# Kernel optimization log

Hardware: AMD Instinct MI355X
Metric: run time of the kernel (lower is better)

Reference implementation:

```python
import jax, jax.numpy as jnp
import numpy as np

B, Q = 4096, 1024   # batch, time-series length
L, K = 64, 32       # num shapelets, shapelet length


def setup_inputs() -> dict:
    key = jax.random.key(0)
    k1, k2, k3, k4 = jax.random.split(key, 4)
    return {
        "ts": jax.random.normal(k1, (B, Q), dtype=jnp.float32),
        "shapelets": jax.random.normal(k2, (L, K), dtype=jnp.float32),
        "fc_w": jax.random.normal(k3, (2, L), dtype=jnp.float32) * 0.1,
        "fc_b": jax.random.normal(k4, (2,), dtype=jnp.float32) * 0.1,
    }


def reference(ts, shapelets, fc_w, fc_b):
    # Sliding-window mean squared distance, fused via the expansion
    #   mean((seg - s)^2) = (sum seg^2 - 2 seg.s + sum s^2) / K
    # which avoids materializing [B, L, S, K] windows.
    S = Q - K + 1  # number of segments

    # sliding sum of ts^2 over windows of length K -> [B, S]
    cs = jnp.concatenate([jnp.zeros((B, 1), ts.dtype), jnp.cumsum(ts * ts, axis=1)], axis=1)
    win_sq = cs[:, K:] - cs[:, :-K]

    # cross-correlation ts * shapelet -> [B, L, S] via a 1D valid conv
    cross = jax.lax.conv_general_dilated(
        ts[:, None, :],          # [B, 1, Q]  (NCW)
        shapelets[:, None, :],   # [L, 1, K]  (OIW)
        window_strides=(1,),
        padding="VALID",
        dimension_numbers=("NCW", "OIW", "NCW"),
    )

    shap_sq = jnp.sum(shapelets * shapelets, axis=1)  # [L]

    # [B, L, S] distance profile, then hard min over segment positions -> [B, L]
    dist = (win_sq[:, None, :] - 2.0 * cross + shap_sq[None, :, None]) / K
    feat = jnp.min(dist, axis=2)

    # fc1
    return feat @ fc_w.T + fc_b
```

## Files before the change

### kernel.cpp

```cpp
#include <hip/hip_runtime.h>
#include <stdint.h>

#define NB 4096
#define QLEN 1024
#define NL 64
#define KLEN 32
#define NS (QLEN - KLEN + 1)

typedef __attribute__((ext_vector_type(8))) _Float16 half8;
typedef __attribute__((ext_vector_type(4))) float f32x4;

union fragh { uint32_t u[4]; half8 v; };

static __device__ __forceinline__ uint32_t pkh(float a, float b) {
    return __builtin_bit_cast(uint32_t, __builtin_amdgcn_cvt_pkrtz(a, b));
}
static __device__ __forceinline__ float lo16f(uint32_t w) {
    return (float)__builtin_bit_cast(_Float16, (unsigned short)(w & 0xFFFFu));
}
static __device__ __forceinline__ float hi16f(uint32_t w) {
    return (float)__builtin_bit_cast(_Float16, (unsigned short)(w >> 16));
}
static __device__ __forceinline__ uint32_t pkh_rne(float a, float b) {
    unsigned short ha = __builtin_bit_cast(unsigned short, (_Float16)a);
    unsigned short hb = __builtin_bit_cast(unsigned short, (_Float16)b);
    return (uint32_t)ha | ((uint32_t)hb << 16);
}

__global__ __launch_bounds__(256, 6) void shapelet_r10(
    const float* __restrict__ ts,
    const float* __restrict__ shapelets,
    const float* __restrict__ fc_w,
    const float* __restrict__ fc_b,
    float* __restrict__ out)
{
    __shared__ __align__(16) uint32_t lds_pkE[544];
    __shared__ __align__(16) uint32_t lds_pkO[544];
    __shared__ __align__(16) uint32_t lds_nwh[512];
    __shared__ __align__(16) float    lds_s4[264];
    __shared__ float lds_ssq[NL];
    __shared__ float lds_pm[4][NL];

    const int tid  = threadIdx.x;
    const int b    = blockIdx.x;
    const int lane = tid & 63;
    const int wave = tid >> 6;
    const int col  = lane & 15;
    const int kg   = lane >> 4;

    float x0, x1, x2;
    {
        float4 v = reinterpret_cast<const float4*>(ts + (size_t)b * QLEN)[tid];
        x0 = v.x; x1 = v.y; x2 = v.z;
        float x3 = v.w;
        float x4g = (tid < 255) ? ts[(size_t)b * QLEN + 4 * tid + 4] : 0.0f;
        uint2 pe = { pkh(x0, x1), pkh(x2, x3) };
        uint2 po = { pkh(x1, x2), pkh(x3, x4g) };
        reinterpret_cast<uint2*>(lds_pkE)[tid] = pe;
        reinterpret_cast<uint2*>(lds_pkO)[tid] = po;
        lds_s4[tid] = fmaf(x0, x0, fmaf(x1, x1, fmaf(x2, x2, x3 * x3)));
    }
    if (tid < 32) { lds_pkE[512 + tid] = 0u; lds_pkO[512 + tid] = 0u; }
    if (tid < 8)  lds_s4[256 + tid] = 0.0f;

    fragh Bh[4];
    #pragma unroll
    for (int lt = 0; lt < 4; ++lt) {
        const float* sp = shapelets + (lt * 16 + col) * KLEN + kg * 8;
        float4 f0 = *reinterpret_cast<const float4*>(sp);
        float4 f1 = *reinterpret_cast<const float4*>(sp + 4);
        Bh[lt].u[0] = pkh(f0.x, f0.y);
        Bh[lt].u[1] = pkh(f0.z, f0.w);
        Bh[lt].u[2] = pkh(f1.x, f1.y);
        Bh[lt].u[3] = pkh(f1.z, f1.w);
    }

    if (tid < NL) {
        const float* sp = shapelets + tid * KLEN;
        float s = 0.0f;
        #pragma unroll
        for (int k = 0; k < KLEN; ++k) s = fmaf(sp[k], sp[k], s);
        lds_ssq[tid] = s;
    }
    __syncthreads();

    {
        float s[8];
        #pragma unroll
        for (int j = 0; j < 8; ++j) s[j] = lds_s4[tid + j];
        float w0 = ((s[0] + s[1]) + (s[2] + s[3])) + ((s[4] + s[5]) + (s[6] + s[7]));
        uint32_t cw0 = lds_pkE[2 * (tid + 8)];
        uint32_t cw1 = lds_pkE[2 * (tid + 8) + 1];
        float x32 = lo16f(cw0), x33 = hi16f(cw0), x34 = lo16f(cw1);
        float w1 = fmaf(x32, x32, fmaf(-x0, x0, w0));
        float w2 = fmaf(x33, x33, fmaf(-x1, x1, w1));
        float w3 = fmaf(x34, x34, fmaf(-x2, x2, w2));
        const int p0 = 4 * tid;
        float c0 = (p0 + 0 < NS) ? -0.5f * w0 : -60000.0f;
        float c1 = (p0 + 1 < NS) ? -0.5f * w1 : -60000.0f;
        float c2 = (p0 + 2 < NS) ? -0.5f * w2 : -60000.0f;
        float c3 = (p0 + 3 < NS) ? -0.5f * w3 : -60000.0f;
        const int q = p0 & 31;
        const int W = ((p0 >> 5) << 4) + (((q & 15) >> 2) << 2) + ((q >> 4) << 1);
        uint2 hw = { pkh_rne(c0, c1), pkh_rne(c2, c3) };
        *reinterpret_cast<uint2*>(&lds_nwh[W]) = hw;
    }
    __syncthreads();

    float rmax[4][4];
    #pragma unroll
    for (int lt = 0; lt < 4; ++lt)
        #pragma unroll
        for (int e = 0; e < 4; ++e) rmax[lt][e] = -3.0e38f;

    const int par = col & 1;
    const uint32_t* apk = par ? lds_pkO : lds_pkE;
    const int abase = ((col - par) >> 1) + kg * 4;
    const int nwb = 4 * kg;

    #pragma unroll 2
    for (int i = 0; i < 8; ++i) {
        const int s0 = 32 * wave + 128 * i;
        const int tp = wave + 4 * i;
        const uint32_t* ap = apk + (s0 >> 1) + abase;
        fragh Aa, Ab;
        #pragma unroll
        for (int j = 0; j < 4; ++j) Aa.u[j] = ap[j];
        #pragma unroll
        for (int j = 0; j < 4; ++j) Ab.u[j] = ap[8 + j];

        uint4 nw = *reinterpret_cast<const uint4*>(&lds_nwh[16 * tp + nwb]);
        f32x4 ia, ib;
        ia[0] = lo16f(nw.x); ia[1] = hi16f(nw.x);
        ia[2] = lo16f(nw.y); ia[3] = hi16f(nw.y);
        ib[0] = lo16f(nw.z); ib[1] = hi16f(nw.z);
        ib[2] = lo16f(nw.w); ib[3] = hi16f(nw.w);

        #pragma unroll
        for (int lt = 0; lt < 4; ++lt) {
            f32x4 aa = __builtin_amdgcn_mfma_f32_16x16x32_f16(Aa.v, Bh[lt].v, ia, 0, 0, 0);
            f32x4 ab = __builtin_amdgcn_mfma_f32_16x16x32_f16(Ab.v, Bh[lt].v, ib, 0, 0, 0);
            #pragma unroll
            for (int e = 0; e < 4; ++e)
                rmax[lt][e] = fmaxf(fmaxf(aa[e], ab[e]), rmax[lt][e]);
        }
    }

    #pragma unroll
    for (int lt = 0; lt < 4; ++lt) {
        float v = fmaxf(fmaxf(rmax[lt][0], rmax[lt][1]),
                        fmaxf(rmax[lt][2], rmax[lt][3]));
        v = fmaxf(v, __shfl_xor(v, 16, 64));
        v = fmaxf(v, __shfl_xor(v, 32, 64));
        if (kg == 0) lds_pm[wave][lt * 16 + col] = v;
    }
    __syncthreads();

    if (wave == 0) {
        float m = fmaxf(fmaxf(lds_pm[0][lane], lds_pm[1][lane]),
                        fmaxf(lds_pm[2][lane], lds_pm[3][lane]));
        float f = (lds_ssq[lane] - 2.0f * m) * (1.0f / (float)KLEN);

        float p0v = f * fc_w[lane];
        float p1v = f * fc_w[NL + lane];
        #pragma unroll
        for (int off = 32; off >= 1; off >>= 1) {
            p0v += __shfl_xor(p0v, off, 64);
            p1v += __shfl_xor(p1v, off, 64);
        }
        if (lane == 0) {
            out[(size_t)b * 2 + 0] = p0v + fc_b[0];
            out[(size_t)b * 2 + 1] = p1v + fc_b[1];
        }
    }
}

extern "C" void kernel_launch(void* const* d_in, const int* in_sizes, int n_in,
                              void* d_out, int out_size, void* d_ws, size_t ws_size,
                              hipStream_t stream) {
    const float* ts        = (const float*)d_in[0];
    const float* shapelets = (const float*)d_in[1];
    const float* fc_w      = (const float*)d_in[2];
    const float* fc_b      = (const float*)d_in[3];
    float* out = (float*)d_out;

    shapelet_r10<<<NB, 256, 0, stream>>>(ts, shapelets, fc_w, fc_b, out);
}
```

Measured before the change: 28.76 us.

## Map one batch row per wave instead of per block, removing block barriers

```diff
diff --git a/kernel.cpp b/kernel.cpp
--- a/kernel.cpp
+++ b/kernel.cpp
@@ -6,6 +6,7 @@
 #define NL 64
 #define KLEN 32
 #define NS (QLEN - KLEN + 1)
+#define WSLICE 1856
 
 typedef __attribute__((ext_vector_type(8))) _Float16 half8;
 typedef __attribute__((ext_vector_type(4))) float f32x4;
@@ -27,43 +28,52 @@
     return (uint32_t)ha | ((uint32_t)hb << 16);
 }
 
-__global__ __launch_bounds__(256, 6) void shapelet_r10(
+__global__ __launch_bounds__(256, 4) void shapelet_r12(
     const float* __restrict__ ts,
     const float* __restrict__ shapelets,
     const float* __restrict__ fc_w,
     const float* __restrict__ fc_b,
     float* __restrict__ out)
 {
-    __shared__ __align__(16) uint32_t lds_pkE[544];
-    __shared__ __align__(16) uint32_t lds_pkO[544];
-    __shared__ __align__(16) uint32_t lds_nwh[512];
-    __shared__ __align__(16) float    lds_s4[264];
-    __shared__ float lds_ssq[NL];
-    __shared__ float lds_pm[4][NL];
+    __shared__ __align__(16) uint32_t lds[4 * WSLICE];
 
     const int tid  = threadIdx.x;
-    const int b    = blockIdx.x;
+    const int wave = tid >> 6;
     const int lane = tid & 63;
-    const int wave = tid >> 6;
     const int col  = lane & 15;
     const int kg   = lane >> 4;
+    const int row  = blockIdx.x * 4 + wave;
 
-    float x0, x1, x2;
-    {
-        float4 v = reinterpret_cast<const float4*>(ts + (size_t)b * QLEN)[tid];
-        x0 = v.x; x1 = v.y; x2 = v.z;
-        float x3 = v.w;
-        float x4g = (tid < 255) ? ts[(size_t)b * QLEN + 4 * tid + 4] : 0.0f;
-        uint2 pe = { pkh(x0, x1), pkh(x2, x3) };
-        uint2 po = { pkh(x1, x2), pkh(x3, x4g) };
-        reinterpret_cast<uint2*>(lds_pkE)[tid] = pe;
-        reinterpret_cast<uint2*>(lds_pkO)[tid] = po;
-        lds_s4[tid] = fmaf(x0, x0, fmaf(x1, x1, fmaf(x2, x2, x3 * x3)));
+    uint32_t* pkE = lds + wave * WSLICE;
+    uint32_t* pkO = pkE + 528;
+    uint32_t* nwh = pkO + 528;
+    float*    s4  = reinterpret_cast<float*>(nwh + 512);
+
+    const float* rowp = ts + (size_t)row * QLEN;
+    float4 v[4];
+    #pragma unroll
+    for (int c = 0; c < 4; ++c)
+        v[c] = reinterpret_cast<const float4*>(rowp)[64 * c + lane];
+    float x4[4];
+    #pragma unroll
+    for (int c = 0; c < 4; ++c) {
+        const int p = 256 * c + 4 * lane + 4;
+        x4[c] = (p < QLEN) ? rowp[p] : 0.0f;
     }
-    if (tid < 32) { lds_pkE[512 + tid] = 0u; lds_pkO[512 + tid] = 0u; }
-    if (tid < 8)  lds_s4[256 + tid] = 0.0f;
+    #pragma unroll
+    for (int c = 0; c < 4; ++c) {
+        uint2 pe = { pkh(v[c].x, v[c].y), pkh(v[c].z, v[c].w) };
+        uint2 po = { pkh(v[c].y, v[c].z), pkh(v[c].w, x4[c]) };
+        reinterpret_cast<uint2*>(pkE)[64 * c + lane] = pe;
+        reinterpret_cast<uint2*>(pkO)[64 * c + lane] = po;
+        s4[64 * c + lane] =
+            fmaf(v[c].x, v[c].x, fmaf(v[c].y, v[c].y, fmaf(v[c].z, v[c].z, v[c].w * v[c].w)));
+    }
+    if (lane < 16) { pkE[512 + lane] = 0u; pkO[512 + lane] = 0u; }
+    if (lane < 8)  s4[256 + lane] = 0.0f;
 
     fragh Bh[4];
+    float ssq[4];
     #pragma unroll
     for (int lt = 0; lt < 4; ++lt) {
         const float* sp = shapelets + (lt * 16 + col) * KLEN + kg * 8;
@@ -73,39 +83,40 @@
         Bh[lt].u[1] = pkh(f0.z, f0.w);
         Bh[lt].u[2] = pkh(f1.x, f1.y);
         Bh[lt].u[3] = pkh(f1.z, f1.w);
+        float s = f0.x * f0.x;
+        s = fmaf(f0.y, f0.y, s); s = fmaf(f0.z, f0.z, s); s = fmaf(f0.w, f0.w, s);
+        s = fmaf(f1.x, f1.x, s); s = fmaf(f1.y, f1.y, s);
+        s = fmaf(f1.z, f1.z, s); s = fmaf(f1.w, f1.w, s);
+        ssq[lt] = s;
     }
 
-    if (tid < NL) {
-        const float* sp = shapelets + tid * KLEN;
-        float s = 0.0f;
+    __builtin_amdgcn_wave_barrier();
+
+    #pragma unroll
+    for (int c = 0; c < 4; ++c) {
+        const int q = 64 * c + lane;
+        float s_[8];
         #pragma unroll
-        for (int k = 0; k < KLEN; ++k) s = fmaf(sp[k], sp[k], s);
-        lds_ssq[tid] = s;
-    }
-    __syncthreads();
-
-    {
-        float s[8];
-        #pragma unroll
-        for (int j = 0; j < 8; ++j) s[j] = lds_s4[tid + j];
-        float w0 = ((s[0] + s[1]) + (s[2] + s[3])) + ((s[4] + s[5]) + (s[6] + s[7]));
-        uint32_t cw0 = lds_pkE[2 * (tid + 8)];
-        uint32_t cw1 = lds_pkE[2 * (tid + 8) + 1];
+        for (int j = 0; j < 8; ++j) s_[j] = s4[q + j];
+        float w0 = ((s_[0] + s_[1]) + (s_[2] + s_[3])) + ((s_[4] + s_[5]) + (s_[6] + s_[7]));
+        uint32_t cw0 = pkE[2 * (q + 8)];
+        uint32_t cw1 = pkE[2 * (q + 8) + 1];
         float x32 = lo16f(cw0), x33 = hi16f(cw0), x34 = lo16f(cw1);
-        float w1 = fmaf(x32, x32, fmaf(-x0, x0, w0));
-        float w2 = fmaf(x33, x33, fmaf(-x1, x1, w1));
-        float w3 = fmaf(x34, x34, fmaf(-x2, x2, w2));
-        const int p0 = 4 * tid;
+        float w1 = fmaf(x32, x32, fmaf(-v[c].x, v[c].x, w0));
+        float w2 = fmaf(x33, x33, fmaf(-v[c].y, v[c].y, w1));
+        float w3 = fmaf(x34, x34, fmaf(-v[c].z, v[c].z, w2));
+        const int p0 = 4 * q;
         float c0 = (p0 + 0 < NS) ? -0.5f * w0 : -60000.0f;
         float c1 = (p0 + 1 < NS) ? -0.5f * w1 : -60000.0f;
         float c2 = (p0 + 2 < NS) ? -0.5f * w2 : -60000.0f;
         float c3 = (p0 + 3 < NS) ? -0.5f * w3 : -60000.0f;
-        const int q = p0 & 31;
-        const int W = ((p0 >> 5) << 4) + (((q & 15) >> 2) << 2) + ((q >> 4) << 1);
+        const int qq = p0 & 31;
+        const int W = ((p0 >> 5) << 4) + (((qq & 15) >> 2) << 2) + ((qq >> 4) << 1);
         uint2 hw = { pkh_rne(c0, c1), pkh_rne(c2, c3) };
-        *reinterpret_cast<uint2*>(&lds_nwh[W]) = hw;
+        *reinterpret_cast<uint2*>(&nwh[W]) = hw;
     }
-    __syncthreads();
+
+    __builtin_amdgcn_wave_barrier();
 
     float rmax[4][4];
     #pragma unroll
@@ -114,22 +125,19 @@
         for (int e = 0; e < 4; ++e) rmax[lt][e] = -3.0e38f;
 
     const int par = col & 1;
-    const uint32_t* apk = par ? lds_pkO : lds_pkE;
-    const int abase = ((col - par) >> 1) + kg * 4;
+    const uint32_t* apk = (par ? pkO : pkE) + (((col - par) >> 1) + kg * 4);
     const int nwb = 4 * kg;
 
     #pragma unroll 2
-    for (int i = 0; i < 8; ++i) {
-        const int s0 = 32 * wave + 128 * i;
-        const int tp = wave + 4 * i;
-        const uint32_t* ap = apk + (s0 >> 1) + abase;
+    for (int i = 0; i < 32; ++i) {
+        const uint32_t* ap = apk + 16 * i;
         fragh Aa, Ab;
         #pragma unroll
         for (int j = 0; j < 4; ++j) Aa.u[j] = ap[j];
         #pragma unroll
         for (int j = 0; j < 4; ++j) Ab.u[j] = ap[8 + j];
 
-        uint4 nw = *reinterpret_cast<const uint4*>(&lds_nwh[16 * tp + nwb]);
+        uint4 nw = *reinterpret_cast<const uint4*>(&nwh[16 * i + nwb]);
         f32x4 ia, ib;
         ia[0] = lo16f(nw.x); ia[1] = hi16f(nw.x);
         ia[2] = lo16f(nw.y); ia[3] = hi16f(nw.y);
@@ -146,32 +154,28 @@
         }
     }
 
+    float p0v = 0.0f, p1v = 0.0f;
     #pragma unroll
     for (int lt = 0; lt < 4; ++lt) {
-        float v = fmaxf(fmaxf(rmax[lt][0], rmax[lt][1]),
+        float m = fmaxf(fmaxf(rmax[lt][0], rmax[lt][1]),
                         fmaxf(rmax[lt][2], rmax[lt][3]));
-        v = fmaxf(v, __shfl_xor(v, 16, 64));
-        v = fmaxf(v, __shfl_xor(v, 32, 64));
-        if (kg == 0) lds_pm[wave][lt * 16 + col] = v;
+        m = fmaxf(m, __shfl_xor(m, 16, 64));
+        m = fmaxf(m, __shfl_xor(m, 32, 64));
+        float sq = ssq[lt];
+        sq += __shfl_xor(sq, 16, 64);
+        sq += __shfl_xor(sq, 32, 64);
+        float f = (sq - 2.0f * m) * (1.0f / (float)KLEN);
+        p0v = fmaf(f, fc_w[lt * 16 + col], p0v);
+        p1v = fmaf(f, fc_w[NL + lt * 16 + col], p1v);
     }
-    __syncthreads();
-
-    if (wave == 0) {
-        float m = fmaxf(fmaxf(lds_pm[0][lane], lds_pm[1][lane]),
-                        fmaxf(lds_pm[2][lane], lds_pm[3][lane]));
-        float f = (lds_ssq[lane] - 2.0f * m) * (1.0f / (float)KLEN);
-
-        float p0v = f * fc_w[lane];
-        float p1v = f * fc_w[NL + lane];
-        #pragma unroll
-        for (int off = 32; off >= 1; off >>= 1) {
-            p0v += __shfl_xor(p0v, off, 64);
-            p1v += __shfl_xor(p1v, off, 64);
-        }
-        if (lane == 0) {
-            out[(size_t)b * 2 + 0] = p0v + fc_b[0];
-            out[(size_t)b * 2 + 1] = p1v + fc_b[1];
-        }
+    #pragma unroll
+    for (int off = 1; off <= 8; off <<= 1) {
+        p0v += __shfl_xor(p0v, off, 64);
+        p1v += __shfl_xor(p1v, off, 64);
+    }
+    if (lane == 0) {
+        out[(size_t)row * 2 + 0] = p0v + fc_b[0];
+        out[(size_t)row * 2 + 1] = p1v + fc_b[1];
     }
 }
 
@@ -184,5 +188,5 @@
     const float* fc_b      = (const float*)d_in[3];
     float* out = (float*)d_out;
 
-    shapelet_r10<<<NB, 256, 0, stream>>>(ts, shapelets, fc_w, fc_b, out);
+    shapelet_r12<<<NB / 4, 256, 0, stream>>>(ts, shapelets, fc_w, fc_b, out);
 }
```

Measured after the change: 23.80 us. -17.3%, faster.
